# Performance work log

Measured on AMD Instinct MI355X. Metric: run time of the kernel, lower is better.

Reference implementation:

```python
import jax, jax.numpy as jnp
import numpy as np

B, S, D, H, FF = 1, 2048, 2048, 32, 8192
HD = D // H
SCALING = HD ** -0.5
WBITS, ABITS = 8, 8
NEG = jnp.finfo(jnp.float32).min


def ste_round(x):
    # straight-through estimator round
    return x + jax.lax.stop_gradient(jnp.round(x) - x)


def fake_quant(x, bits, axis):
    # min-max asymmetric fake quantization (OmniQuant-style dynamic quant)
    qmax = float(2 ** bits - 1)
    xmin = jnp.minimum(jnp.min(x, axis=axis, keepdims=True), 0.0)
    xmax = jnp.maximum(jnp.max(x, axis=axis, keepdims=True), 0.0)
    scale = jnp.maximum((xmax - xmin) / qmax, 1e-5)
    zp = jnp.round(-xmin / scale)
    q = jnp.clip(ste_round(x / scale) + zp, 0.0, qmax)
    return (q - zp) * scale


def qlinear(x, W, b):
    # QuantLinear: quantize activation per-token, weight per-output-channel
    xq = fake_quant(x, ABITS, -1)
    Wq = fake_quant(W, WBITS, 1)  # W: [out, in], per-row (output channel)
    return xq @ Wq.T + b


def layernorm(x, g, b):
    mu = jnp.mean(x, axis=-1, keepdims=True)
    var = jnp.var(x, axis=-1, keepdims=True)
    return (x - mu) * jax.lax.rsqrt(var + 1e-5) * g + b


def setup_inputs():
    key = jax.random.key(0)
    ks = jax.random.split(key, 16)
    w = lambda k, shape: (jax.random.normal(k, shape) * 0.02).astype(jnp.float32)
    hidden_states = jax.random.normal(ks[0], (B, S, D), dtype=jnp.float32)
    causal = jnp.tril(jnp.ones((S, S), dtype=bool))
    attention_mask = jnp.where(causal, 0.0, NEG)[None, None].astype(jnp.float32)
    attention_mask = jnp.broadcast_to(attention_mask, (B, 1, S, S))
    return {
        'hidden_states': hidden_states,
        'attention_mask': attention_mask,
        'Wq': w(ks[1], (D, D)), 'bq': jnp.zeros((D,), jnp.float32),
        'Wk': w(ks[2], (D, D)), 'bk': jnp.zeros((D,), jnp.float32),
        'Wv': w(ks[3], (D, D)), 'bv': jnp.zeros((D,), jnp.float32),
        'Wo': w(ks[4], (D, D)), 'bo': jnp.zeros((D,), jnp.float32),
        'ln1_g': jnp.ones((D,), jnp.float32), 'ln1_b': jnp.zeros((D,), jnp.float32),
        'W1': w(ks[5], (FF, D)), 'b1': jnp.zeros((FF,), jnp.float32),
        'W2': w(ks[6], (D, FF)), 'b2': jnp.zeros((D,), jnp.float32),
        'ln2_g': jnp.ones((D,), jnp.float32), 'ln2_b': jnp.zeros((D,), jnp.float32),
    }


def _split_heads(x):
    # [B,S,D] -> [B,H,S,HD]
    return x.reshape(B, S, H, HD).transpose(0, 2, 1, 3)


def _layer(hidden_states, attention_mask, Wq, bq, Wk, bk, Wv, bv, Wo, bo,
           ln1_g, ln1_b, W1, b1, W2, b2, ln2_g, ln2_b):
    # ---- self attention block (do_layer_norm_before=True) ----
    residual = hidden_states
    x = layernorm(hidden_states, ln1_g, ln1_b)

    q = qlinear(x, Wq, bq) * SCALING
    q = fake_quant(q, ABITS, -1)          # qkt_matmul.quant_x1
    k = qlinear(x, Wk, bk)
    k = fake_quant(k, ABITS, -1)          # qkt_matmul.quant_x2
    v = qlinear(x, Wv, bv)
    v = fake_quant(v, ABITS, -1)          # pv_matmul.quant_x2

    qh, kh, vh = _split_heads(q), _split_heads(k), _split_heads(v)
    scores = jnp.einsum('bhqd,bhkd->bhqk', qh, kh)  # [B,H,S,S]
    scores = scores + attention_mask
    scores = jnp.maximum(scores, NEG)
    probs = jax.nn.softmax(scores, axis=-1)
    probs = fake_quant(probs, ABITS, -1)  # pv_matmul.quant_x1
    ctx = jnp.einsum('bhqk,bhkd->bhqd', probs, vh)
    ctx = ctx.transpose(0, 2, 1, 3).reshape(B, S, D)
    attn_out = qlinear(ctx, Wo, bo)
    hidden_states = residual + attn_out

    # ---- FFN block ----
    residual = hidden_states
    x = layernorm(hidden_states, ln2_g, ln2_b)
    x = jax.nn.relu(qlinear(x, W1, b1))
    x = qlinear(x, W2, b2)
    return residual + x


def reference(hidden_states, attention_mask, Wq, bq, Wk, bk, Wv, bv, Wo, bo,
              ln1_g, ln1_b, W1, b1, W2, b2, ln2_g, ln2_b):
    return _layer(hidden_states, attention_mask, Wq, bq, Wk, bk, Wv, bv, Wo, bo,
                  ln1_g, ln1_b, W1, b1, W2, b2, ln2_g, ln2_b)
```

## Files before the change

### kernel.cpp

```cpp
#include <hip/hip_runtime.h>
#include <hip/hip_bf16.h>
#include <math.h>

#define S_LEN 2048
#define D_DIM 2048
#define H_NUM 32
#define HD_DIM 64
#define FF_DIM 8192
#define QMAX 255.0f

typedef __attribute__((ext_vector_type(4))) float f32x4;
typedef __attribute__((ext_vector_type(4))) int i32x4;
typedef __attribute__((ext_vector_type(8))) __bf16 bf16x8;
typedef unsigned short u16;
typedef signed char i8;

__device__ __forceinline__ u16 f32i_to_bf16(float v) {
  return (u16)(__float_as_uint(v) >> 16);
}
__device__ __forceinline__ u16 f32_to_bf16_rne(float v) {
  __bf16 b = (__bf16)v;
  return *(u16*)&b;
}
__device__ __forceinline__ float bf16_to_f32(u16 u) {
  return __uint_as_float((unsigned int)u << 16);
}
__device__ __forceinline__ int pack4_i8(float q0, float q1, float q2, float q3) {
  int c0 = (int)q0 - 128, c1 = (int)q1 - 128, c2 = (int)q2 - 128, c3 = (int)q3 - 128;
  return (c0 & 0xFF) | ((c1 & 0xFF) << 8) | ((c2 & 0xFF) << 16) | ((c3 & 0xFF) << 24);
}

__device__ __forceinline__ float wred_sum(float v) {
#pragma unroll
  for (int o = 1; o < 64; o <<= 1) v += __shfl_xor(v, o, 64);
  return v;
}
__device__ __forceinline__ float wred_min(float v) {
#pragma unroll
  for (int o = 1; o < 64; o <<= 1) v = fminf(v, __shfl_xor(v, o, 64));
  return v;
}
__device__ __forceinline__ float wred_max(float v) {
#pragma unroll
  for (int o = 1; o < 64; o <<= 1) v = fmaxf(v, __shfl_xor(v, o, 64));
  return v;
}

__device__ __forceinline__ void gload_lds16(const void* g, void* l) {
  __builtin_amdgcn_global_load_lds(
      (__attribute__((address_space(1))) void*)(g),
      (__attribute__((address_space(3))) void*)(l), 16, 0, 0);
}

__device__ __forceinline__ void xcd_swz(int& bx, int& by) {
  const int gx = gridDim.x;
  const int nwg = gx * gridDim.y;
  const int orig = blockIdx.x + gx * blockIdx.y;
  const int swz = (orig & 7) * (nwg >> 3) + (orig >> 3);
  bx = swz % gx;
  by = swz / gx;
}

__global__ __launch_bounds__(256) void ln_quant_i8(const float* __restrict__ x,
                                                   const float* __restrict__ g,
                                                   const float* __restrict__ bvec,
                                                   i8* __restrict__ out,
                                                   float* __restrict__ srow,
                                                   float* __restrict__ zrow,
                                                   float* __restrict__ S0row,
                                                   float* __restrict__ S1row) {
  __shared__ float red[8];
  const int row = blockIdx.x, tid = threadIdx.x;
  const float4* xr = (const float4*)(x + (size_t)row * D_DIM);
  const float4* g4 = (const float4*)g;
  const float4* b4 = (const float4*)bvec;

  float4 v0 = xr[tid], v1 = xr[tid + 256];
  float s = v0.x + v0.y + v0.z + v0.w + v1.x + v1.y + v1.z + v1.w;
  float ss = v0.x * v0.x + v0.y * v0.y + v0.z * v0.z + v0.w * v0.w +
             v1.x * v1.x + v1.y * v1.y + v1.z * v1.z + v1.w * v1.w;
  s = wred_sum(s); ss = wred_sum(ss);
  if ((tid & 63) == 0) { red[tid >> 6] = s; red[4 + (tid >> 6)] = ss; }
  __syncthreads();
  float mu = (red[0] + red[1] + red[2] + red[3]) / (float)D_DIM;
  float var = (red[4] + red[5] + red[6] + red[7]) / (float)D_DIM - mu * mu;
  float rstd = 1.0f / sqrtf(var + 1e-5f);
  __syncthreads();

  float mn = 0.f, mx = 0.f;
  float4 n0, n1;
  {
    float4 gg = g4[tid], bb = b4[tid];
    n0.x = (v0.x - mu) * rstd * gg.x + bb.x; n0.y = (v0.y - mu) * rstd * gg.y + bb.y;
    n0.z = (v0.z - mu) * rstd * gg.z + bb.z; n0.w = (v0.w - mu) * rstd * gg.w + bb.w;
    gg = g4[tid + 256]; bb = b4[tid + 256];
    n1.x = (v1.x - mu) * rstd * gg.x + bb.x; n1.y = (v1.y - mu) * rstd * gg.y + bb.y;
    n1.z = (v1.z - mu) * rstd * gg.z + bb.z; n1.w = (v1.w - mu) * rstd * gg.w + bb.w;
    mn = fminf(mn, fminf(fminf(n0.x, n0.y), fminf(n0.z, n0.w)));
    mn = fminf(mn, fminf(fminf(n1.x, n1.y), fminf(n1.z, n1.w)));
    mx = fmaxf(mx, fmaxf(fmaxf(n0.x, n0.y), fmaxf(n0.z, n0.w)));
    mx = fmaxf(mx, fmaxf(fmaxf(n1.x, n1.y), fmaxf(n1.z, n1.w)));
  }
  mn = wred_min(mn); mx = wred_max(mx);
  if ((tid & 63) == 0) { red[tid >> 6] = mn; red[4 + (tid >> 6)] = mx; }
  __syncthreads();
  mn = fminf(fminf(red[0], red[1]), fminf(red[2], red[3]));
  mx = fmaxf(fmaxf(red[4], red[5]), fmaxf(red[6], red[7]));
  float scale = fmaxf((mx - mn) / QMAX, 1e-5f);
  float zp = rintf(-mn / scale);
  if (tid == 0) { srow[row] = scale; zrow[row] = 128.0f - zp; }

  float q00 = fminf(fmaxf(rintf(n0.x / scale) + zp, 0.f), QMAX);
  float q01 = fminf(fmaxf(rintf(n0.y / scale) + zp, 0.f), QMAX);
  float q02 = fminf(fmaxf(rintf(n0.z / scale) + zp, 0.f), QMAX);
  float q03 = fminf(fmaxf(rintf(n0.w / scale) + zp, 0.f), QMAX);
  float q10 = fminf(fmaxf(rintf(n1.x / scale) + zp, 0.f), QMAX);
  float q11 = fminf(fmaxf(rintf(n1.y / scale) + zp, 0.f), QMAX);
  float q12 = fminf(fmaxf(rintf(n1.z / scale) + zp, 0.f), QMAX);
  float q13 = fminf(fmaxf(rintf(n1.w / scale) + zp, 0.f), QMAX);
  *(int*)&out[(size_t)row * D_DIM + tid * 4] = pack4_i8(q00, q01, q02, q03);
  *(int*)&out[(size_t)row * D_DIM + 1024 + tid * 4] = pack4_i8(q10, q11, q12, q13);
  float s0 = q00 + q01 + q02 + q03 - 512.f;
  float s1 = q10 + q11 + q12 + q13 - 512.f;
  __syncthreads();
  s0 = wred_sum(s0); s1 = wred_sum(s1);
  if ((tid & 63) == 0) { red[tid >> 6] = s0; red[4 + (tid >> 6)] = s1; }
  __syncthreads();
  if (tid == 0) {
    S0row[row] = red[0] + red[1] + red[2] + red[3];
    S1row[row] = red[4] + red[5] + red[6] + red[7];
  }
}

__global__ __launch_bounds__(256) void act_quant_i8(const float* __restrict__ x,
                                                    i8* __restrict__ out,
                                                    float* __restrict__ srow,
                                                    float* __restrict__ zrow,
                                                    float* __restrict__ S0row,
                                                    float* __restrict__ S1row) {
  __shared__ float red[8];
  const int row = blockIdx.x, tid = threadIdx.x;
  const float4* xr = (const float4*)(x + (size_t)row * D_DIM);
  float4 n0 = xr[tid], n1 = xr[tid + 256];
  float mn = 0.f, mx = 0.f;
  mn = fminf(mn, fminf(fminf(n0.x, n0.y), fminf(n0.z, n0.w)));
  mn = fminf(mn, fminf(fminf(n1.x, n1.y), fminf(n1.z, n1.w)));
  mx = fmaxf(mx, fmaxf(fmaxf(n0.x, n0.y), fmaxf(n0.z, n0.w)));
  mx = fmaxf(mx, fmaxf(fmaxf(n1.x, n1.y), fmaxf(n1.z, n1.w)));
  mn = wred_min(mn); mx = wred_max(mx);
  if ((tid & 63) == 0) { red[tid >> 6] = mn; red[4 + (tid >> 6)] = mx; }
  __syncthreads();
  mn = fminf(fminf(red[0], red[1]), fminf(red[2], red[3]));
  mx = fmaxf(fmaxf(red[4], red[5]), fmaxf(red[6], red[7]));
  float scale = fmaxf((mx - mn) / QMAX, 1e-5f);
  float zp = rintf(-mn / scale);
  if (tid == 0) { srow[row] = scale; zrow[row] = 128.0f - zp; }
  float q00 = fminf(fmaxf(rintf(n0.x / scale) + zp, 0.f), QMAX);
  float q01 = fminf(fmaxf(rintf(n0.y / scale) + zp, 0.f), QMAX);
  float q02 = fminf(fmaxf(rintf(n0.z / scale) + zp, 0.f), QMAX);
  float q03 = fminf(fmaxf(rintf(n0.w / scale) + zp, 0.f), QMAX);
  float q10 = fminf(fmaxf(rintf(n1.x / scale) + zp, 0.f), QMAX);
  float q11 = fminf(fmaxf(rintf(n1.y / scale) + zp, 0.f), QMAX);
  float q12 = fminf(fmaxf(rintf(n1.z / scale) + zp, 0.f), QMAX);
  float q13 = fminf(fmaxf(rintf(n1.w / scale) + zp, 0.f), QMAX);
  *(int*)&out[(size_t)row * D_DIM + tid * 4] = pack4_i8(q00, q01, q02, q03);
  *(int*)&out[(size_t)row * D_DIM + 1024 + tid * 4] = pack4_i8(q10, q11, q12, q13);
  float s0 = q00 + q01 + q02 + q03 - 512.f;
  float s1 = q10 + q11 + q12 + q13 - 512.f;
  __syncthreads();
  s0 = wred_sum(s0); s1 = wred_sum(s1);
  if ((tid & 63) == 0) { red[tid >> 6] = s0; red[4 + (tid >> 6)] = s1; }
  __syncthreads();
  if (tid == 0) {
    S0row[row] = red[0] + red[1] + red[2] + red[3];
    S1row[row] = red[4] + red[5] + red[6] + red[7];
  }
}

__device__ __forceinline__ void wquant_body(const float* __restrict__ wr0,
                                            i8* __restrict__ wo,
                                            float* __restrict__ sc,
                                            float* __restrict__ zc,
                                            float* __restrict__ S0c,
                                            float* __restrict__ S1c,
                                            int row, int K) {
  __shared__ float red[8];
  const int tid = threadIdx.x;
  const float4* wr = (const float4*)wr0;
  const int K4 = K >> 2, H4 = K4 >> 1;
  float mn = 0.f, mx = 0.f;
  for (int i = tid; i < K4; i += 256) {
    float4 v = wr[i];
    mn = fminf(mn, fminf(fminf(v.x, v.y), fminf(v.z, v.w)));
    mx = fmaxf(mx, fmaxf(fmaxf(v.x, v.y), fmaxf(v.z, v.w)));
  }
  mn = wred_min(mn); mx = wred_max(mx);
  if ((tid & 63) == 0) { red[tid >> 6] = mn; red[4 + (tid >> 6)] = mx; }
  __syncthreads();
  mn = fminf(fminf(red[0], red[1]), fminf(red[2], red[3]));
  mx = fmaxf(fmaxf(red[4], red[5]), fmaxf(red[6], red[7]));
  float scale = fmaxf((mx - mn) / QMAX, 1e-5f);
  float zp = rintf(-mn / scale);
  if (tid == 0) { sc[row] = scale; zc[row] = 128.0f - zp; }
  float s0 = 0.f, s1 = 0.f;
  for (int i = tid; i < K4; i += 256) {
    float4 v = wr[i];
    float q0 = fminf(fmaxf(rintf(v.x / scale) + zp, 0.f), QMAX);
    float q1 = fminf(fmaxf(rintf(v.y / scale) + zp, 0.f), QMAX);
    float q2 = fminf(fmaxf(rintf(v.z / scale) + zp, 0.f), QMAX);
    float q3 = fminf(fmaxf(rintf(v.w / scale) + zp, 0.f), QMAX);
    *(int*)&wo[i * 4] = pack4_i8(q0, q1, q2, q3);
    float gs = q0 + q1 + q2 + q3 - 512.f;
    if (i < H4) s0 += gs; else s1 += gs;
  }
  __syncthreads();
  s0 = wred_sum(s0); s1 = wred_sum(s1);
  if ((tid & 63) == 0) { red[tid >> 6] = s0; red[4 + (tid >> 6)] = s1; }
  __syncthreads();
  if (tid == 0) {
    S0c[row] = red[0] + red[1] + red[2] + red[3];
    S1c[row] = red[4] + red[5] + red[6] + red[7];
  }
}

__global__ __launch_bounds__(256) void wquant_i8(const float* __restrict__ W,
                                                 i8* __restrict__ Wi,
                                                 float* __restrict__ sc,
                                                 float* __restrict__ zc,
                                                 float* __restrict__ S0c,
                                                 float* __restrict__ S1c, int K) {
  const int row = blockIdx.x;
  wquant_body(W + (size_t)row * K, Wi + (size_t)row * K, sc, zc, S0c, S1c, row, K);
}

__global__ __launch_bounds__(256) void wquant4_i8(
    const float* __restrict__ W0, i8* __restrict__ O0, float* s0, float* z0, float* a0, float* b0,
    const float* __restrict__ W1, i8* __restrict__ O1, float* s1, float* z1, float* a1, float* b1,
    const float* __restrict__ W2, i8* __restrict__ O2, float* s2, float* z2, float* a2, float* b2,
    const float* __restrict__ W3, i8* __restrict__ O3, float* s3, float* z3, float* a3, float* b3) {
  const int which = blockIdx.x >> 11;
  const int row = blockIdx.x & (D_DIM - 1);
  const float* W = (which == 0) ? W0 : (which == 1) ? W1 : (which == 2) ? W2 : W3;
  i8* O = (which == 0) ? O0 : (which == 1) ? O1 : (which == 2) ? O2 : O3;
  float* sc = (which == 0) ? s0 : (which == 1) ? s1 : (which == 2) ? s2 : s3;
  float* zc = (which == 0) ? z0 : (which == 1) ? z1 : (which == 2) ? z2 : z3;
  float* Sa = (which == 0) ? a0 : (which == 1) ? a1 : (which == 2) ? a2 : a3;
  float* Sb = (which == 0) ? b0 : (which == 1) ? b1 : (which == 2) ? b2 : b3;
  wquant_body(W + (size_t)row * D_DIM, O + (size_t)row * D_DIM, sc, zc, Sa, Sb, row, D_DIM);
}

__global__ __launch_bounds__(256) void requant3(
    const u16* __restrict__ qv, const float* __restrict__ tqmn, const float* __restrict__ tqmx,
    u16* __restrict__ qo, float* __restrict__ sqv,
    const u16* __restrict__ kv, const float* __restrict__ tkmn, const float* __restrict__ tkmx,
    u16* __restrict__ ko, float* __restrict__ skv,
    const u16* __restrict__ vv, const float* __restrict__ tvmn, const float* __restrict__ tvmx,
    u16* __restrict__ vo) {
  __shared__ float red[8];
  const int wh = blockIdx.x >> 11;
  const int row = blockIdx.x & (S_LEN - 1);
  const int tid = threadIdx.x;
  const u16* vals = (wh == 0) ? qv : (wh == 1) ? kv : vv;
  const float* tmn = (wh == 0) ? tqmn : (wh == 1) ? tkmn : tvmn;
  const float* tmx = (wh == 0) ? tqmx : (wh == 1) ? tkmx : tvmx;
  u16* out = (wh == 0) ? qo : (wh == 1) ? ko : vo;
  float* srow = (wh == 0) ? sqv : (wh == 1) ? skv : nullptr;
  const int value_mode = (wh == 2) ? 1 : 0;

  float mn = 0.f, mx = 0.f;
  if (tid < 32) {
    mn = tmn[(size_t)row * 32 + tid];
    mx = tmx[(size_t)row * 32 + tid];
  }
  mn = wred_min(mn); mx = wred_max(mx);
  if ((tid & 63) == 0) { red[tid >> 6] = mn; red[4 + (tid >> 6)] = mx; }
  __syncthreads();
  mn = fminf(fminf(red[0], red[1]), fminf(red[2], red[3]));
  mx = fmaxf(fmaxf(red[4], red[5]), fmaxf(red[6], red[7]));
  mn = fminf(mn, 0.f); mx = fmaxf(mx, 0.f);
  float scale = fmaxf((mx - mn) / QMAX, 1e-5f);
  float zp = rintf(-mn / scale);
  if (srow && tid == 0) srow[row] = scale;
  const ushort4* vr = (const ushort4*)(vals + (size_t)row * D_DIM);
  ushort4* orow = (ushort4*)(out + (size_t)row * D_DIM);
  for (int i = tid; i < D_DIM / 4; i += 256) {
    ushort4 u = vr[i];
    float q0 = fminf(fmaxf(rintf(bf16_to_f32(u.x) / scale) + zp, 0.f), QMAX) - zp;
    float q1 = fminf(fmaxf(rintf(bf16_to_f32(u.y) / scale) + zp, 0.f), QMAX) - zp;
    float q2 = fminf(fmaxf(rintf(bf16_to_f32(u.z) / scale) + zp, 0.f), QMAX) - zp;
    float q3 = fminf(fmaxf(rintf(bf16_to_f32(u.w) / scale) + zp, 0.f), QMAX) - zp;
    ushort4 o;
    if (value_mode) {
      o.x = f32_to_bf16_rne(q0 * scale); o.y = f32_to_bf16_rne(q1 * scale);
      o.z = f32_to_bf16_rne(q2 * scale); o.w = f32_to_bf16_rne(q3 * scale);
    } else {
      o.x = f32i_to_bf16(q0); o.y = f32i_to_bf16(q1);
      o.z = f32i_to_bf16(q2); o.w = f32i_to_bf16(q3);
    }
    orow[i] = o;
  }
}

__global__ __launch_bounds__(256) void requant_ff_i8(const u16* __restrict__ vals,
                                                     const float* __restrict__ tmx,
                                                     i8* __restrict__ out,
                                                     float* __restrict__ srow,
                                                     float* __restrict__ zrow,
                                                     float* __restrict__ S0row,
                                                     float* __restrict__ S1row) {
  __shared__ float red[8];
  const int row = blockIdx.x, tid = threadIdx.x;
  float mx = (tid < 128) ? tmx[(size_t)row * 128 + tid] : 0.f;
  mx = wred_max(mx);
  if ((tid & 63) == 0) red[tid >> 6] = mx;
  __syncthreads();
  mx = fmaxf(fmaxf(red[0], red[1]), fmaxf(red[2], red[3]));
  mx = fmaxf(mx, 0.f);
  float scale = fmaxf(mx / QMAX, 1e-5f);
  if (tid == 0) { srow[row] = scale; zrow[row] = 128.0f; }
  const ushort4* vr = (const ushort4*)(vals + (size_t)row * FF_DIM);
  const int N4 = FF_DIM >> 2;
  float s0 = 0.f, s1 = 0.f;
  for (int i = tid; i < N4; i += 256) {
    ushort4 u = vr[i];
    float q0 = fminf(fmaxf(rintf(bf16_to_f32(u.x) / scale), 0.f), QMAX);
    float q1 = fminf(fmaxf(rintf(bf16_to_f32(u.y) / scale), 0.f), QMAX);
    float q2 = fminf(fmaxf(rintf(bf16_to_f32(u.z) / scale), 0.f), QMAX);
    float q3 = fminf(fmaxf(rintf(bf16_to_f32(u.w) / scale), 0.f), QMAX);
    *(int*)&out[(size_t)row * FF_DIM + i * 4] = pack4_i8(q0, q1, q2, q3);
    float gs = q0 + q1 + q2 + q3 - 512.f;
    if (i < 1024) s0 += gs; else s1 += gs;
  }
  __syncthreads();
  s0 = wred_sum(s0); s1 = wred_sum(s1);
  if ((tid & 63) == 0) { red[tid >> 6] = s0; red[4 + (tid >> 6)] = s1; }
  __syncthreads();
  if (tid == 0) {
    S0row[row] = red[0] + red[1] + red[2] + red[3];
    S1row[row] = red[4] + red[5] + red[6] + red[7];
  }
}

__device__ __forceinline__ void gemm128_i8_db(
    const i8* __restrict__ A, const i8* __restrict__ B,
    int K, int bm, int bn, int k_begin, int k_end,
    i8* As, i8* Bs, i32x4 (&acc)[4][4]) {
  const int tid = threadIdx.x;
  const int wid = tid >> 6, lane = tid & 63;
  const int wr = wid >> 1, wc = wid & 1;
  const int lr = lane & 15, lk = lane >> 4;
  const int r0 = tid >> 2, c0 = (tid & 3) * 16;
  const int r1 = 64 + r0;
  const size_t ldsb0 = (size_t)(wid * 64) * 16;
  const size_t ldsb1 = (size_t)(256 + wid * 64) * 16;

  const i8* Ag0 = A + (size_t)(bm + r0) * K + c0;
  const i8* Ag1 = A + (size_t)(bm + r1) * K + c0;
  const i8* Bg0 = B + (size_t)(bn + r0) * K + c0;
  const i8* Bg1 = B + (size_t)(bn + r1) * K + c0;

  const int nt = (k_end - k_begin) >> 6;

#define STAGE_I8(t)                                   \
  {                                                   \
    const int _k = k_begin + (t) * 64;                \
    i8* _Ab = As + (size_t)((t) & 1) * 8192;          \
    i8* _Bb = Bs + (size_t)((t) & 1) * 8192;          \
    gload_lds16(Ag0 + _k, _Ab + ldsb0);               \
    gload_lds16(Ag1 + _k, _Ab + ldsb1);               \
    gload_lds16(Bg0 + _k, _Bb + ldsb0);               \
    gload_lds16(Bg1 + _k, _Bb + ldsb1);               \
  }

  STAGE_I8(0);
  __syncthreads();

  for (int t = 0; t < nt; ++t) {
    const i8* Ac = As + (size_t)(t & 1) * 8192;
    const i8* Bc = Bs + (size_t)(t & 1) * 8192;
    i32x4 af[4], bf[4];
#pragma unroll
    for (int mi = 0; mi < 4; ++mi)
      af[mi] = *(const i32x4*)&Ac[(size_t)(wr * 64 + mi * 16 + lr) * 64 + lk * 16];
#pragma unroll
    for (int ni = 0; ni < 4; ++ni)
      bf[ni] = *(const i32x4*)&Bc[(size_t)(wc * 64 + ni * 16 + lr) * 64 + lk * 16];
    if (t + 1 < nt) STAGE_I8(t + 1);
#pragma unroll
    for (int mi = 0; mi < 4; ++mi)
#pragma unroll
      for (int ni = 0; ni < 4; ++ni)
        acc[mi][ni] = __builtin_amdgcn_mfma_i32_16x16x64_i8(af[mi], bf[ni], acc[mi][ni], 0, 0, 0);
    __syncthreads();
  }
#undef STAGE_I8
}

__global__ __launch_bounds__(256) void gemm_qkv_i8(
    const i8* __restrict__ A, const float* __restrict__ sx, const float* __restrict__ zx,
    const float* __restrict__ Sx0, const float* __restrict__ Sx1,
    const i8* __restrict__ Bq, const float* __restrict__ sbq, const float* __restrict__ zbq,
    const float* __restrict__ Sq0, const float* __restrict__ Sq1,
    const float* __restrict__ biasq, u16* __restrict__ Cq,
    float* __restrict__ tqmn, float* __restrict__ tqmx,
    const i8* __restrict__ Bk, const float* __restrict__ sbk, const float* __restrict__ zbk,
    const float* __restrict__ Sk0, const float* __restrict__ Sk1,
    const float* __restrict__ biask, u16* __restrict__ Ck,
    float* __restrict__ tkmn, float* __restrict__ tkmx,
    const i8* __restrict__ Bv, const float* __restrict__ sbv, const float* __restrict__ zbv,
    const float* __restrict__ Sv0, const float* __restrict__ Sv1,
    const float* __restrict__ biasv, u16* __restrict__ Cv,
    float* __restrict__ tvmn, float* __restrict__ tvmx) {
  __shared__ __align__(16) i8 As[2 * 128 * 64], Bs[2 * 128 * 64];
  int bx, by; xcd_swz(bx, by);
  const int which = bx >> 4;
  const int bn = (bx & 15) * 128;
  const int bm = by * 128;
  const i8* B = (which == 0) ? Bq : (which == 1) ? Bk : Bv;
  const float* sb = (which == 0) ? sbq : (which == 1) ? sbk : sbv;
  const float* zb = (which == 0) ? zbq : (which == 1) ? zbk : zbv;
  const float* Sb0 = (which == 0) ? Sq0 : (which == 1) ? Sk0 : Sv0;
  const float* Sb1 = (which == 0) ? Sq1 : (which == 1) ? Sk1 : Sv1;
  const float* bias = (which == 0) ? biasq : (which == 1) ? biask : biasv;
  u16* C = (which == 0) ? Cq : (which == 1) ? Ck : Cv;
  float* tmn = (which == 0) ? tqmn : (which == 1) ? tkmn : tvmn;
  float* tmx = (which == 0) ? tqmx : (which == 1) ? tkmx : tvmx;
  const float alpha = (which == 0) ? 0.125f : 1.0f;

  i32x4 acc[4][4] = {};
  gemm128_i8_db(A, B, D_DIM, bm, bn, 0, D_DIM, As, Bs, acc);

  const int tid = threadIdx.x;
  const int wid = tid >> 6, lane = tid & 63;
  const int wr = wid >> 1, wc = wid & 1;
  const int lr = lane & 15, lk = lane >> 4;
  const int col0 = bn + wc * 64 + lr;
  const int rbase = bm + wr * 64 + lk * 4;
  const int tci = (bn >> 6) + wc;
  float sbc[4], zbc[4], Sbc[4], bc[4];
#pragma unroll
  for (int ni = 0; ni < 4; ++ni) {
    const int col = col0 + ni * 16;
    sbc[ni] = sb[col]; zbc[ni] = zb[col];
    Sbc[ni] = Sb0[col] + Sb1[col]; bc[ni] = bias[col];
  }
#pragma unroll
  for (int mi = 0; mi < 4; ++mi) {
#pragma unroll
    for (int r = 0; r < 4; ++r) {
      const int row = rbase + mi * 16 + r;
      const float sar = sx[row], zar = zx[row];
      const float Sar = Sx0[row] + Sx1[row];
// ... 99 lines not shown
#pragma unroll
    for (int mi = 0; mi < 4; ++mi)
#pragma unroll
      for (int r = 0; r < 4; ++r)
        dst[(size_t)(rbase + mi * 16 + r) * D_DIM + col] = (float)acc[mi][ni][r];
  }
}

__global__ __launch_bounds__(256) void splitk_reduce4(
    const float* __restrict__ part,
    const float* __restrict__ sxa, const float* __restrict__ zxa,
    const float* __restrict__ Sxa0, const float* __restrict__ Sxa1,
    const float* __restrict__ sw, const float* __restrict__ zw,
    const float* __restrict__ Sw0, const float* __restrict__ Sw1,
    float Kf, const float* __restrict__ bias, const float* __restrict__ res,
    float* __restrict__ out) {
  const size_t st4 = (size_t)S_LEN * D_DIM / 4;
  for (size_t i = (size_t)blockIdx.x * 256 + threadIdx.x; i < st4;
       i += (size_t)gridDim.x * 256) {
    const int row = (int)(i >> 9);
    const int c4 = (int)(i & 511);
    float4 s = ((const float4*)part)[i];
    float4 p1 = ((const float4*)part)[i + st4];
    float4 p2 = ((const float4*)part)[i + 2 * st4];
    float4 p3 = ((const float4*)part)[i + 3 * st4];
    s.x += p1.x + p2.x + p3.x; s.y += p1.y + p2.y + p3.y;
    s.z += p1.z + p2.z + p3.z; s.w += p1.w + p2.w + p3.w;
    const float sxr = sxa[row], zxr = zxa[row];
    const float Sxr = Sxa0[row] + Sxa1[row];
    float4 ws = ((const float4*)sw)[c4];
    float4 wz = ((const float4*)zw)[c4];
    float4 w0 = ((const float4*)Sw0)[c4];
    float4 w1 = ((const float4*)Sw1)[c4];
    float4 b4 = ((const float4*)bias)[c4];
    float4 o;
    o.x = sxr * ws.x * (s.x + zxr * (w0.x + w1.x) + wz.x * Sxr + Kf * zxr * wz.x) + b4.x;
    o.y = sxr * ws.y * (s.y + zxr * (w0.y + w1.y) + wz.y * Sxr + Kf * zxr * wz.y) + b4.y;
    o.z = sxr * ws.z * (s.z + zxr * (w0.z + w1.z) + wz.z * Sxr + Kf * zxr * wz.z) + b4.z;
    o.w = sxr * ws.w * (s.w + zxr * (w0.w + w1.w) + wz.w * Sxr + Kf * zxr * wz.w) + b4.w;
    if (res) {
      float4 r = ((const float4*)res)[i];
      o.x += r.x; o.y += r.y; o.z += r.z; o.w += r.w;
    }
    ((float4*)out)[i] = o;
  }
}

__global__ __launch_bounds__(256) void splitk_reduce_ln(
    const float* __restrict__ part,
    const float* __restrict__ sxa, const float* __restrict__ zxa,
    const float* __restrict__ Sxa0, const float* __restrict__ Sxa1,
    const float* __restrict__ sw, const float* __restrict__ zw,
    const float* __restrict__ Sw0, const float* __restrict__ Sw1,
    const float* __restrict__ bias, const float* __restrict__ res,
    float* __restrict__ h2out,
    const float* __restrict__ g, const float* __restrict__ bvec,
    i8* __restrict__ out, float* __restrict__ srow, float* __restrict__ zrow,
    float* __restrict__ S0row, float* __restrict__ S1row) {
  __shared__ float red[8];
  const int row = blockIdx.x, tid = threadIdx.x;
  const size_t st = (size_t)S_LEN * D_DIM;
  const float4* p0 = (const float4*)(part + (size_t)row * D_DIM);
  const float4* p1 = (const float4*)(part + st + (size_t)row * D_DIM);
  const float4* p2 = (const float4*)(part + 2 * st + (size_t)row * D_DIM);
  const float4* p3 = (const float4*)(part + 3 * st + (size_t)row * D_DIM);
  const float4* rr = (const float4*)(res + (size_t)row * D_DIM);
  const float4* b4 = (const float4*)bias;
  const float4* g4 = (const float4*)g;
  const float4* e4 = (const float4*)bvec;

  const float sxr = sxa[row], zxr = zxa[row];
  const float Sxr = Sxa0[row] + Sxa1[row];

  float4 v0, v1;
#pragma unroll
  for (int h = 0; h < 2; ++h) {
    const int idx = tid + h * 256;
    float4 a = p0[idx], q = p1[idx], u = p2[idx], w = p3[idx];
    float4 ws = ((const float4*)sw)[idx];
    float4 wz = ((const float4*)zw)[idx];
    float4 s0 = ((const float4*)Sw0)[idx];
    float4 s1 = ((const float4*)Sw1)[idx];
    float4 bb = b4[idx], rv = rr[idx];
    float4 o;
    o.x = sxr * ws.x * (a.x + q.x + u.x + w.x + zxr * (s0.x + s1.x) + wz.x * Sxr + 2048.0f * zxr * wz.x) + bb.x + rv.x;
    o.y = sxr * ws.y * (a.y + q.y + u.y + w.y + zxr * (s0.y + s1.y) + wz.y * Sxr + 2048.0f * zxr * wz.y) + bb.y + rv.y;
    o.z = sxr * ws.z * (a.z + q.z + u.z + w.z + zxr * (s0.z + s1.z) + wz.z * Sxr + 2048.0f * zxr * wz.z) + bb.z + rv.z;
    o.w = sxr * ws.w * (a.w + q.w + u.w + w.w + zxr * (s0.w + s1.w) + wz.w * Sxr + 2048.0f * zxr * wz.w) + bb.w + rv.w;
    if (h == 0) v0 = o; else v1 = o;
  }
  float* h2r = h2out + (size_t)row * D_DIM;
  *(float4*)&h2r[tid * 4] = v0;
  *(float4*)&h2r[1024 + tid * 4] = v1;

  float s = v0.x + v0.y + v0.z + v0.w + v1.x + v1.y + v1.z + v1.w;
  float ss = v0.x * v0.x + v0.y * v0.y + v0.z * v0.z + v0.w * v0.w +
             v1.x * v1.x + v1.y * v1.y + v1.z * v1.z + v1.w * v1.w;
  s = wred_sum(s); ss = wred_sum(ss);
  if ((tid & 63) == 0) { red[tid >> 6] = s; red[4 + (tid >> 6)] = ss; }
  __syncthreads();
  float mu = (red[0] + red[1] + red[2] + red[3]) / (float)D_DIM;
  float var = (red[4] + red[5] + red[6] + red[7]) / (float)D_DIM - mu * mu;
  float rstd = 1.0f / sqrtf(var + 1e-5f);
  __syncthreads();

  float mn = 0.f, mx = 0.f;
  float4 n0, n1;
  {
    float4 gg = g4[tid], bb = e4[tid];
    n0.x = (v0.x - mu) * rstd * gg.x + bb.x; n0.y = (v0.y - mu) * rstd * gg.y + bb.y;
    n0.z = (v0.z - mu) * rstd * gg.z + bb.z; n0.w = (v0.w - mu) * rstd * gg.w + bb.w;
    gg = g4[tid + 256]; bb = e4[tid + 256];
    n1.x = (v1.x - mu) * rstd * gg.x + bb.x; n1.y = (v1.y - mu) * rstd * gg.y + bb.y;
    n1.z = (v1.z - mu) * rstd * gg.z + bb.z; n1.w = (v1.w - mu) * rstd * gg.w + bb.w;
    mn = fminf(mn, fminf(fminf(n0.x, n0.y), fminf(n0.z, n0.w)));
    mn = fminf(mn, fminf(fminf(n1.x, n1.y), fminf(n1.z, n1.w)));
    mx = fmaxf(mx, fmaxf(fmaxf(n0.x, n0.y), fmaxf(n0.z, n0.w)));
    mx = fmaxf(mx, fmaxf(fmaxf(n1.x, n1.y), fmaxf(n1.z, n1.w)));
  }
  mn = wred_min(mn); mx = wred_max(mx);
  if ((tid & 63) == 0) { red[tid >> 6] = mn; red[4 + (tid >> 6)] = mx; }
  __syncthreads();
  mn = fminf(fminf(red[0], red[1]), fminf(red[2], red[3]));
  mx = fmaxf(fmaxf(red[4], red[5]), fmaxf(red[6], red[7]));
  float scale = fmaxf((mx - mn) / QMAX, 1e-5f);
  float zp = rintf(-mn / scale);
  if (tid == 0) { srow[row] = scale; zrow[row] = 128.0f - zp; }
  float q00 = fminf(fmaxf(rintf(n0.x / scale) + zp, 0.f), QMAX);
  float q01 = fminf(fmaxf(rintf(n0.y / scale) + zp, 0.f), QMAX);
  float q02 = fminf(fmaxf(rintf(n0.z / scale) + zp, 0.f), QMAX);
  float q03 = fminf(fmaxf(rintf(n0.w / scale) + zp, 0.f), QMAX);
  float q10 = fminf(fmaxf(rintf(n1.x / scale) + zp, 0.f), QMAX);
  float q11 = fminf(fmaxf(rintf(n1.y / scale) + zp, 0.f), QMAX);
  float q12 = fminf(fmaxf(rintf(n1.z / scale) + zp, 0.f), QMAX);
  float q13 = fminf(fmaxf(rintf(n1.w / scale) + zp, 0.f), QMAX);
  *(int*)&out[(size_t)row * D_DIM + tid * 4] = pack4_i8(q00, q01, q02, q03);
  *(int*)&out[(size_t)row * D_DIM + 1024 + tid * 4] = pack4_i8(q10, q11, q12, q13);
  float s0 = q00 + q01 + q02 + q03 - 512.f;
  float s1 = q10 + q11 + q12 + q13 - 512.f;
  __syncthreads();
  s0 = wred_sum(s0); s1 = wred_sum(s1);
  if ((tid & 63) == 0) { red[tid >> 6] = s0; red[4 + (tid >> 6)] = s1; }
  __syncthreads();
  if (tid == 0) {
    S0row[row] = red[0] + red[1] + red[2] + red[3];
    S1row[row] = red[4] + red[5] + red[6] + red[7];
  }
}

__global__ __launch_bounds__(256) void attn_ml(
    const u16* __restrict__ qi, const float* __restrict__ sq,
    const u16* __restrict__ ki, const float* __restrict__ sk,
    float* __restrict__ Mb, float* __restrict__ Lb) {
  __shared__ __align__(16) u16 Qs[64][72];
  __shared__ __align__(16) u16 Ks[64][72];
  const int bid = blockIdx.x;
  const int ti = (S_LEN / 64 - 1) - (bid >> 5);
  const int h = bid & (H_NUM - 1);
  const int i0 = ti * 64;
  const int tid = threadIdx.x;
  const int wid = tid >> 6, lane = tid & 63;
  const int lr = lane & 15, g = lane >> 4;
  const size_t hbase = (size_t)h * HD_DIM;

  const int r_a = tid >> 3, ch_a = tid & 7;
  const int r_b = 32 + r_a;

  for (int c = tid; c < 512; c += 256) {
    int r = c >> 3, ch = c & 7;
    *(float4*)&Qs[r][ch * 8] =
        *(const float4*)&qi[(size_t)(i0 + r) * D_DIM + hbase + ch * 8];
  }
  float sq4[4];
#pragma unroll
  for (int r = 0; r < 4; ++r) sq4[r] = sq[i0 + wid * 16 + g * 4 + r];
  __syncthreads();

  const int ntiles = i0 / 64 + 1;
  float m_r[4] = {-1e30f, -1e30f, -1e30f, -1e30f};
  float l_r[4] = {0.f, 0.f, 0.f, 0.f};

  float4 ka0 = *(const float4*)&ki[(size_t)r_a * D_DIM + hbase + ch_a * 8];
  float4 ka1 = *(const float4*)&ki[(size_t)r_b * D_DIM + hbase + ch_a * 8];
  for (int t = 0; t < ntiles; ++t) {
    __syncthreads();
    *(float4*)&Ks[r_a][ch_a * 8] = ka0;
    *(float4*)&Ks[r_b][ch_a * 8] = ka1;
    __syncthreads();
    if (t + 1 < ntiles) {
      const int jn = (t + 1) * 64;
      ka0 = *(const float4*)&ki[(size_t)(jn + r_a) * D_DIM + hbase + ch_a * 8];
      ka1 = *(const float4*)&ki[(size_t)(jn + r_b) * D_DIM + hbase + ch_a * 8];
    }

    bf16x8 aq0 = *(const bf16x8*)&Qs[wid * 16 + lr][g * 8];
    bf16x8 aq1 = *(const bf16x8*)&Qs[wid * 16 + lr][32 + g * 8];
    f32x4 accs[4] = {};
#pragma unroll
    for (int ni = 0; ni < 4; ++ni) {
      bf16x8 b0 = *(const bf16x8*)&Ks[ni * 16 + lr][g * 8];
      bf16x8 b1 = *(const bf16x8*)&Ks[ni * 16 + lr][32 + g * 8];
      accs[ni] = __builtin_amdgcn_mfma_f32_16x16x32_bf16(aq0, b0, accs[ni], 0, 0, 0);
      accs[ni] = __builtin_amdgcn_mfma_f32_16x16x32_bf16(aq1, b1, accs[ni], 0, 0, 0);
    }

    const int jt = t * 64;
    float sv[4][4];
#pragma unroll
    for (int ni = 0; ni < 4; ++ni) {
      const float skc = sk[jt + ni * 16 + lr];
#pragma unroll
      for (int r = 0; r < 4; ++r) sv[ni][r] = accs[ni][r] * sq4[r] * skc;
    }
    if (t == ntiles - 1) {
      const int jcol = jt + lr, irow = i0 + wid * 16 + g * 4;
#pragma unroll
      for (int ni = 0; ni < 4; ++ni)
#pragma unroll
        for (int r = 0; r < 4; ++r)
          if (jcol + ni * 16 > irow + r) sv[ni][r] = -1e30f;
    }
#pragma unroll
    for (int r = 0; r < 4; ++r) {
      float tmax = fmaxf(fmaxf(sv[0][r], sv[1][r]), fmaxf(sv[2][r], sv[3][r]));
      tmax = fmaxf(tmax, __shfl_xor(tmax, 1, 64));
      tmax = fmaxf(tmax, __shfl_xor(tmax, 2, 64));
      tmax = fmaxf(tmax, __shfl_xor(tmax, 4, 64));
      tmax = fmaxf(tmax, __shfl_xor(tmax, 8, 64));
      float mnew = fmaxf(m_r[r], tmax);
      float sum = __expf(sv[0][r] - mnew) + __expf(sv[1][r] - mnew) +
                  __expf(sv[2][r] - mnew) + __expf(sv[3][r] - mnew);
      sum += __shfl_xor(sum, 1, 64);
      sum += __shfl_xor(sum, 2, 64);
      sum += __shfl_xor(sum, 4, 64);
      sum += __shfl_xor(sum, 8, 64);
      l_r[r] = l_r[r] * __expf(m_r[r] - mnew) + sum;
      m_r[r] = mnew;
    }
  }

  if (lr == 0) {
#pragma unroll
    for (int r = 0; r < 4; ++r) {
      const int row = i0 + wid * 16 + g * 4 + r;
      Mb[(size_t)h * S_LEN + row] = m_r[r];
      Lb[(size_t)h * S_LEN + row] = l_r[r];
    }
  }
}

__global__ __launch_bounds__(256) void attn_pv(
    const u16* __restrict__ qi, const float* __restrict__ sq,
    const u16* __restrict__ ki, const float* __restrict__ sk,
    const u16* __restrict__ vf,
    const float* __restrict__ Mb, const float* __restrict__ Lb,
    float* __restrict__ ctx) {
  __shared__ __align__(16) u16 Qs[64][72];
  __shared__ __align__(16) u16 Ks[64][72];
  __shared__ __align__(16) u16 Ps[64][72];
  __shared__ __align__(16) u16 Vt[64][72];
  const int bid = blockIdx.x;
  const int ti = (S_LEN / 64 - 1) - (bid >> 5);
  const int h = bid & (H_NUM - 1);
  const int i0 = ti * 64;
  const int tid = threadIdx.x;
  const int wid = tid >> 6, lane = tid & 63;
  const int lr = lane & 15, g = lane >> 4;
  const size_t hbase = (size_t)h * HD_DIM;

  const int r_a = tid >> 3, ch_a = tid & 7;
  const int r_b = 32 + r_a;
  const int jr_v = tid & 63, ch_v = tid >> 6;

  for (int c = tid; c < 512; c += 256) {
    int r = c >> 3, ch = c & 7;
    *(float4*)&Qs[r][ch * 8] =
        *(const float4*)&qi[(size_t)(i0 + r) * D_DIM + hbase + ch * 8];
  }
  float sq4[4], m_r[4], qsc[4], idn[4];
#pragma unroll
  for (int r = 0; r < 4; ++r) {
    const int row = i0 + wid * 16 + g * 4 + r;
    sq4[r] = sq[row];
    m_r[r] = Mb[(size_t)h * S_LEN + row];
    float li = Lb[(size_t)h * S_LEN + row];
    float sc = fmaxf((1.0f / li) / QMAX, 1e-5f);
    qsc[r] = sc;
    idn[r] = 1.0f / (li * sc);
  }
  __syncthreads();

  const int ntiles = i0 / 64 + 1;
  f32x4 acco[4] = {};
  float4 kb0 = *(const float4*)&ki[(size_t)r_a * D_DIM + hbase + ch_a * 8];
  float4 kb1 = *(const float4*)&ki[(size_t)r_b * D_DIM + hbase + ch_a * 8];
  float4 vb0 = *(const float4*)&vf[(size_t)jr_v * D_DIM + hbase + ch_v * 8];
  float4 vb1 = *(const float4*)&vf[(size_t)jr_v * D_DIM + hbase + (4 + ch_v) * 8];
  for (int t = 0; t < ntiles; ++t) {
    __syncthreads();
    *(float4*)&Ks[r_a][ch_a * 8] = kb0;
    *(float4*)&Ks[r_b][ch_a * 8] = kb1;
    {
      const u16* v0 = (const u16*)&vb0;
      const u16* v1 = (const u16*)&vb1;
#pragma unroll
      for (int e = 0; e < 8; ++e) Vt[ch_v * 8 + e][jr_v] = v0[e];
#pragma unroll
      for (int e = 0; e < 8; ++e) Vt[(4 + ch_v) * 8 + e][jr_v] = v1[e];
    }
    __syncthreads();
    if (t + 1 < ntiles) {
      const int jn = (t + 1) * 64;
      kb0 = *(const float4*)&ki[(size_t)(jn + r_a) * D_DIM + hbase + ch_a * 8];
      kb1 = *(const float4*)&ki[(size_t)(jn + r_b) * D_DIM + hbase + ch_a * 8];
      vb0 = *(const float4*)&vf[(size_t)(jn + jr_v) * D_DIM + hbase + ch_v * 8];
      vb1 = *(const float4*)&vf[(size_t)(jn + jr_v) * D_DIM + hbase + (4 + ch_v) * 8];
    }

    bf16x8 aq0 = *(const bf16x8*)&Qs[wid * 16 + lr][g * 8];
    bf16x8 aq1 = *(const bf16x8*)&Qs[wid * 16 + lr][32 + g * 8];
    f32x4 accs[4] = {};
#pragma unroll
    for (int ni = 0; ni < 4; ++ni) {
      bf16x8 b0 = *(const bf16x8*)&Ks[ni * 16 + lr][g * 8];
      bf16x8 b1 = *(const bf16x8*)&Ks[ni * 16 + lr][32 + g * 8];
      accs[ni] = __builtin_amdgcn_mfma_f32_16x16x32_bf16(aq0, b0, accs[ni], 0, 0, 0);
      accs[ni] = __builtin_amdgcn_mfma_f32_16x16x32_bf16(aq1, b1, accs[ni], 0, 0, 0);
    }

    const int jt = t * 64;
    const bool diag = (t == ntiles - 1);
    const int jcol = jt + lr, irow = i0 + wid * 16 + g * 4;
#pragma unroll
    for (int ni = 0; ni < 4; ++ni) {
      const float skc = sk[jt + ni * 16 + lr];
#pragma unroll
      for (int r = 0; r < 4; ++r) {
        float s = accs[ni][r] * sq4[r] * skc;
        if (diag && (jcol + ni * 16 > irow + r)) s = -1e30f;
        float e = __expf(s - m_r[r]);
        float q8 = fminf(fmaxf(rintf(e * idn[r]), 0.f), QMAX);
        Ps[wid * 16 + g * 4 + r][ni * 16 + lr] = f32i_to_bf16(q8);
      }
    }

    bf16x8 ap0 = *(const bf16x8*)&Ps[wid * 16 + lr][g * 8];
    bf16x8 ap1 = *(const bf16x8*)&Ps[wid * 16 + lr][32 + g * 8];
#pragma unroll
    for (int ni = 0; ni < 4; ++ni) {
      bf16x8 b0 = *(const bf16x8*)&Vt[ni * 16 + lr][g * 8];
      bf16x8 b1 = *(const bf16x8*)&Vt[ni * 16 + lr][32 + g * 8];
      acco[ni] = __builtin_amdgcn_mfma_f32_16x16x32_bf16(ap0, b0, acco[ni], 0, 0, 0);
      acco[ni] = __builtin_amdgcn_mfma_f32_16x16x32_bf16(ap1, b1, acco[ni], 0, 0, 0);
    }
  }

#pragma unroll
  for (int ni = 0; ni < 4; ++ni)
#pragma unroll
    for (int r = 0; r < 4; ++r) {
      const int row = i0 + wid * 16 + g * 4 + r;
      ctx[(size_t)row * D_DIM + hbase + ni * 16 + lr] = acco[ni][r] * qsc[r];
    }
}

extern "C" void kernel_launch(void* const* d_in, const int* in_sizes, int n_in,
                              void* d_out, int out_size, void* d_ws, size_t ws_size,
                              hipStream_t stream) {
  (void)in_sizes; (void)n_in; (void)out_size;
  const float* hs  = (const float*)d_in[0];
  const float* Wq  = (const float*)d_in[2];
  const float* bq  = (const float*)d_in[3];
  const float* Wk  = (const float*)d_in[4];
  const float* bk  = (const float*)d_in[5];
  const float* Wv  = (const float*)d_in[6];
  const float* bv  = (const float*)d_in[7];
  const float* Wo  = (const float*)d_in[8];
  const float* bo  = (const float*)d_in[9];
  const float* g1  = (const float*)d_in[10];
  const float* be1 = (const float*)d_in[11];
  const float* W1  = (const float*)d_in[12];
  const float* bf1 = (const float*)d_in[13];
  const float* W2  = (const float*)d_in[14];
  const float* bf2 = (const float*)d_in[15];
  const float* g2  = (const float*)d_in[16];
  const float* be2 = (const float*)d_in[17];
  float* out = (float*)d_out;

  const size_t SD = (size_t)S_LEN * D_DIM;
  const size_t SF = (size_t)S_LEN * FF_DIM;
  const size_t HS = (size_t)H_NUM * S_LEN;

  char* p = (char*)d_ws;
  auto alloc = [&](size_t bytes) { char* r = p; p += (bytes + 255) & ~(size_t)255; return r; };

  float* h2   = (float*)alloc(SD * 4);
  float* sx   = (float*)alloc(S_LEN * 4);
  float* zx   = (float*)alloc(S_LEN * 4);
  float* Sx0  = (float*)alloc(S_LEN * 4);
  float* Sx1  = (float*)alloc(S_LEN * 4);
  float* sy   = (float*)alloc(S_LEN * 4);
  float* zy   = (float*)alloc(S_LEN * 4);
  float* Sy0  = (float*)alloc(S_LEN * 4);
  float* Sy1  = (float*)alloc(S_LEN * 4);
  float* sxf  = (float*)alloc(S_LEN * 4);
  float* zxf  = (float*)alloc(S_LEN * 4);
  float* Sf0  = (float*)alloc(S_LEN * 4);
  float* Sf1  = (float*)alloc(S_LEN * 4);
  float* sqv  = (float*)alloc(S_LEN * 4);
  float* skv  = (float*)alloc(S_LEN * 4);
  float* Mb   = (float*)alloc(HS * 4);
  float* Lbv  = (float*)alloc(HS * 4);
  float* swq = (float*)alloc(D_DIM * 4); float* zwq = (float*)alloc(D_DIM * 4);
  float* Sq0 = (float*)alloc(D_DIM * 4); float* Sq1 = (float*)alloc(D_DIM * 4);
  float* swk = (float*)alloc(D_DIM * 4); float* zwk = (float*)alloc(D_DIM * 4);
  float* Sk0 = (float*)alloc(D_DIM * 4); float* Sk1 = (float*)alloc(D_DIM * 4);
  float* swv = (float*)alloc(D_DIM * 4); float* zwv = (float*)alloc(D_DIM * 4);
  float* Sv0 = (float*)alloc(D_DIM * 4); float* Sv1 = (float*)alloc(D_DIM * 4);
  float* swo = (float*)alloc(D_DIM * 4); float* zwo = (float*)alloc(D_DIM * 4);
  float* So0 = (float*)alloc(D_DIM * 4); float* So1 = (float*)alloc(D_DIM * 4);
  float* sw1 = (float*)alloc(FF_DIM * 4); float* zw1 = (float*)alloc(FF_DIM * 4);
  float* S10 = (float*)alloc(FF_DIM * 4); float* S11 = (float*)alloc(FF_DIM * 4);
  float* sw2 = (float*)alloc(D_DIM * 4); float* zw2 = (float*)alloc(D_DIM * 4);
  float* S20 = (float*)alloc(D_DIM * 4); float* S21 = (float*)alloc(D_DIM * 4);
  float* tqmn = (float*)alloc(S_LEN * 32 * 4);
  float* tqmx = (float*)alloc(S_LEN * 32 * 4);
  float* tkmn = (float*)alloc(S_LEN * 32 * 4);
  float* tkmx = (float*)alloc(S_LEN * 32 * 4);
  float* tvmn = (float*)alloc(S_LEN * 32 * 4);
  float* tvmx = (float*)alloc(S_LEN * 32 * 4);
  float* tf1x = (float*)alloc(S_LEN * 128 * 4);
  i8* xi  = (i8*)alloc(SD);
  i8* wqi = (i8*)alloc(SD);
  i8* wki = (i8*)alloc(SD);
  i8* wvi = (i8*)alloc(SD);
  i8* woi = (i8*)alloc(SD);
  i8* w1i = (i8*)alloc(SF);
  i8* w2i = (i8*)alloc(SF);
  i8* f1i = (i8*)alloc(SF);
  char* arena = alloc(8 * SD * 2);
  u16* qv   = (u16*)arena;
  u16* kv   = qv + SD;
  u16* vv   = kv + SD;
  u16* qi8  = vv + SD;
  u16* ki8  = qi8 + SD;
  u16* vfb  = ki8 + SD;
  float* ctxb = (float*)(vfb + SD);
  float* pwo = (float*)arena;
  u16* f1v = (u16*)arena;
  float* pw2 = (float*)arena;
  size_t need = (size_t)(p - (char*)d_ws);
  if (ws_size < need) return;

  dim3 blk(256);

  wquant4_i8<<<4 * D_DIM, blk, 0, stream>>>(
      Wq, wqi, swq, zwq, Sq0, Sq1,
      Wk, wki, swk, zwk, Sk0, Sk1,
      Wv, wvi, swv, zwv, Sv0, Sv1,
      Wo, woi, swo, zwo, So0, So1);
  wquant_i8<<<FF_DIM, blk, 0, stream>>>(W1, w1i, sw1, zw1, S10, S11, D_DIM);
  wquant_i8<<<D_DIM, blk, 0, stream>>>(W2, w2i, sw2, zw2, S20, S21, FF_DIM);

  ln_quant_i8<<<S_LEN, blk, 0, stream>>>(hs, g1, be1, xi, sx, zx, Sx0, Sx1);

  dim3 gqkv(3 * D_DIM / 128, S_LEN / 128);
  gemm_qkv_i8<<<gqkv, blk, 0, stream>>>(xi, sx, zx, Sx0, Sx1,
                                        wqi, swq, zwq, Sq0, Sq1, bq, qv, tqmn, tqmx,
                                        wki, swk, zwk, Sk0, Sk1, bk, kv, tkmn, tkmx,
                                        wvi, swv, zwv, Sv0, Sv1, bv, vv, tvmn, tvmx);

  requant3<<<3 * S_LEN, blk, 0, stream>>>(qv, tqmn, tqmx, qi8, sqv,
                                          kv, tkmn, tkmx, ki8, skv,
                                          vv, tvmn, tvmx, vfb);

  const int ga = (S_LEN / 64) * H_NUM;
  attn_ml<<<ga, blk, 0, stream>>>(qi8, sqv, ki8, skv, Mb, Lbv);
  attn_pv<<<ga, blk, 0, stream>>>(qi8, sqv, ki8, skv, vfb, Mb, Lbv, ctxb);

  act_quant_i8<<<S_LEN, blk, 0, stream>>>(ctxb, xi, sx, zx, Sx0, Sx1);

  dim3 gwo(D_DIM / 128, S_LEN / 128, 4);
  gemm_splitk_i8<<<gwo, blk, 0, stream>>>(xi, woi, pwo, D_DIM, 4);
  splitk_reduce_ln<<<S_LEN, blk, 0, stream>>>(pwo, sx, zx, Sx0, Sx1,
                                              swo, zwo, So0, So1, bo, hs, h2,
                                              g2, be2, xi, sy, zy, Sy0, Sy1);

  dim3 gff(FF_DIM / 128, S_LEN / 128);
  gemm_w1_i8<<<gff, blk, 0, stream>>>(xi, sy, zy, Sy0, Sy1,
                                      w1i, sw1, zw1, S10, S11, bf1, f1v, tf1x);
  requant_ff_i8<<<S_LEN, blk, 0, stream>>>(f1v, tf1x, f1i, sxf, zxf, Sf0, Sf1);

  dim3 gw2(D_DIM / 128, S_LEN / 128, 4);
  gemm_splitk_i8<<<gw2, blk, 0, stream>>>(f1i, w2i, pw2, FF_DIM, 4);
  splitk_reduce4<<<2048, blk, 0, stream>>>(pw2, sxf, zxf, Sf0, Sf1,
                                           sw2, zw2, S20, S21, (float)FF_DIM,
                                           bf2, h2, out);
}
```

Before: 421.1 us.

## Pre-transpose V, load Q fragments directly, and use exp2 with folded scales in attention

Adds a separate kernel that transposes the quantized V into a head-major [d][seq] buffer. attn_pv can then fill its Vt shared tile with vectorized stores instead of scattered 2-byte writes. Q fragments are read straight from global into registers, which drops the Qs shared tile and a barrier. The softmax now uses exp2f with log2e folded into the query scale, and the probability normalization is folded into a per-row bias. The cost is an extra kernel launch and a full pass over V, plus small rounding differences from the exp2 rewrite.

```diff
diff --git a/kernel.cpp b/kernel.cpp
--- a/kernel.cpp
+++ b/kernel.cpp
@@ -8,6 +8,7 @@
 #define HD_DIM 64
 #define FF_DIM 8192
 #define QMAX 255.0f
+#define LOG2E 1.4426950408889634f
 
 typedef __attribute__((ext_vector_type(4))) float f32x4;
 typedef __attribute__((ext_vector_type(4))) int i32x4;
@@ -298,6 +299,27 @@
       o.z = f32i_to_bf16(q2); o.w = f32i_to_bf16(q3);
     }
     orow[i] = o;
+  }
+}
+
+__global__ __launch_bounds__(256) void transpose_v(const u16* __restrict__ vfb,
+                                                   u16* __restrict__ vtb) {
+  __shared__ u16 Ts[64][66];
+  const int j0 = blockIdx.x * 64;
+  const int h = blockIdx.y;
+  const int tid = threadIdx.x;
+  for (int c = tid; c < 512; c += 256) {
+    int r = c >> 3, ch = c & 7;
+    *(float4*)&Ts[r][ch * 8] =
+        *(const float4*)&vfb[(size_t)(j0 + r) * D_DIM + h * HD_DIM + ch * 8];
+  }
+  __syncthreads();
+  for (int c = tid; c < 512; c += 256) {
+    int d = c >> 3, ch = c & 7;
+    u16 tmp[8];
+#pragma unroll
+    for (int e = 0; e < 8; ++e) tmp[e] = Ts[ch * 8 + e][d];
+    *(float4*)&vtb[(size_t)(h * HD_DIM + d) * S_LEN + j0 + ch * 8] = *(float4*)tmp;
   }
 }
 
@@ -703,7 +725,6 @@
     const u16* __restrict__ qi, const float* __restrict__ sq,
     const u16* __restrict__ ki, const float* __restrict__ sk,
     float* __restrict__ Mb, float* __restrict__ Lb) {
-  __shared__ __align__(16) u16 Qs[64][72];
   __shared__ __align__(16) u16 Ks[64][72];
   const int bid = blockIdx.x;
   const int ti = (S_LEN / 64 - 1) - (bid >> 5);
@@ -717,15 +738,11 @@
   const int r_a = tid >> 3, ch_a = tid & 7;
   const int r_b = 32 + r_a;
 
-  for (int c = tid; c < 512; c += 256) {
-    int r = c >> 3, ch = c & 7;
-    *(float4*)&Qs[r][ch * 8] =
-        *(const float4*)&qi[(size_t)(i0 + r) * D_DIM + hbase + ch * 8];
-  }
-  float sq4[4];
-#pragma unroll
-  for (int r = 0; r < 4; ++r) sq4[r] = sq[i0 + wid * 16 + g * 4 + r];
-  __syncthreads();
+  const bf16x8 aq0 = *(const bf16x8*)&qi[(size_t)(i0 + wid * 16 + lr) * D_DIM + hbase + g * 8];
+  const bf16x8 aq1 = *(const bf16x8*)&qi[(size_t)(i0 + wid * 16 + lr) * D_DIM + hbase + 32 + g * 8];
+  float sq2[4];
+#pragma unroll
+  for (int r = 0; r < 4; ++r) sq2[r] = sq[i0 + wid * 16 + g * 4 + r] * LOG2E;
 
   const int ntiles = i0 / 64 + 1;
   float m_r[4] = {-1e30f, -1e30f, -1e30f, -1e30f};
@@ -744,8 +761,6 @@
       ka1 = *(const float4*)&ki[(size_t)(jn + r_b) * D_DIM + hbase + ch_a * 8];
     }
 
-    bf16x8 aq0 = *(const bf16x8*)&Qs[wid * 16 + lr][g * 8];
-    bf16x8 aq1 = *(const bf16x8*)&Qs[wid * 16 + lr][32 + g * 8];
     f32x4 accs[4] = {};
 #pragma unroll
     for (int ni = 0; ni < 4; ++ni) {
@@ -756,12 +771,12 @@
     }
 
     const int jt = t * 64;
-    float sv[4][4];
+    float tv[4][4];
 #pragma unroll
     for (int ni = 0; ni < 4; ++ni) {
       const float skc = sk[jt + ni * 16 + lr];
 #pragma unroll
-      for (int r = 0; r < 4; ++r) sv[ni][r] = accs[ni][r] * sq4[r] * skc;
+      for (int r = 0; r < 4; ++r) tv[ni][r] = accs[ni][r] * sq2[r] * skc;
     }
     if (t == ntiles - 1) {
       const int jcol = jt + lr, irow = i0 + wid * 16 + g * 4;
@@ -769,23 +784,23 @@
       for (int ni = 0; ni < 4; ++ni)
 #pragma unroll
         for (int r = 0; r < 4; ++r)
-          if (jcol + ni * 16 > irow + r) sv[ni][r] = -1e30f;
+          if (jcol + ni * 16 > irow + r) tv[ni][r] = -1e30f;
     }
 #pragma unroll
     for (int r = 0; r < 4; ++r) {
-      float tmax = fmaxf(fmaxf(sv[0][r], sv[1][r]), fmaxf(sv[2][r], sv[3][r]));
+      float tmax = fmaxf(fmaxf(tv[0][r], tv[1][r]), fmaxf(tv[2][r], tv[3][r]));
       tmax = fmaxf(tmax, __shfl_xor(tmax, 1, 64));
       tmax = fmaxf(tmax, __shfl_xor(tmax, 2, 64));
       tmax = fmaxf(tmax, __shfl_xor(tmax, 4, 64));
       tmax = fmaxf(tmax, __shfl_xor(tmax, 8, 64));
       float mnew = fmaxf(m_r[r], tmax);
-      float sum = __expf(sv[0][r] - mnew) + __expf(sv[1][r] - mnew) +
-                  __expf(sv[2][r] - mnew) + __expf(sv[3][r] - mnew);
+      float sum = exp2f(tv[0][r] - mnew) + exp2f(tv[1][r] - mnew) +
+                  exp2f(tv[2][r] - mnew) + exp2f(tv[3][r] - mnew);
       sum += __shfl_xor(sum, 1, 64);
       sum += __shfl_xor(sum, 2, 64);
       sum += __shfl_xor(sum, 4, 64);
       sum += __shfl_xor(sum, 8, 64);
-      l_r[r] = l_r[r] * __expf(m_r[r] - mnew) + sum;
+      l_r[r] = l_r[r] * exp2f(m_r[r] - mnew) + sum;
       m_r[r] = mnew;
     }
   }
@@ -803,10 +818,9 @@
 __global__ __launch_bounds__(256) void attn_pv(
     const u16* __restrict__ qi, const float* __restrict__ sq,
     const u16* __restrict__ ki, const float* __restrict__ sk,
-    const u16* __restrict__ vf,
+    const u16* __restrict__ vt,
     const float* __restrict__ Mb, const float* __restrict__ Lb,
     float* __restrict__ ctx) {
-  __shared__ __align__(16) u16 Qs[64][72];
   __shared__ __align__(16) u16 Ks[64][72];
   __shared__ __align__(16) u16 Ps[64][72];
   __shared__ __align__(16) u16 Vt[64][72];
@@ -818,58 +832,47 @@
   const int wid = tid >> 6, lane = tid & 63;
   const int lr = lane & 15, g = lane >> 4;
   const size_t hbase = (size_t)h * HD_DIM;
+  const size_t vtbase = (size_t)h * HD_DIM * S_LEN;
 
   const int r_a = tid >> 3, ch_a = tid & 7;
   const int r_b = 32 + r_a;
-  const int jr_v = tid & 63, ch_v = tid >> 6;
-
-  for (int c = tid; c < 512; c += 256) {
-    int r = c >> 3, ch = c & 7;
-    *(float4*)&Qs[r][ch * 8] =
-        *(const float4*)&qi[(size_t)(i0 + r) * D_DIM + hbase + ch * 8];
-  }
-  float sq4[4], m_r[4], qsc[4], idn[4];
+
+  const bf16x8 aq0 = *(const bf16x8*)&qi[(size_t)(i0 + wid * 16 + lr) * D_DIM + hbase + g * 8];
+  const bf16x8 aq1 = *(const bf16x8*)&qi[(size_t)(i0 + wid * 16 + lr) * D_DIM + hbase + 32 + g * 8];
+
+  float sq2[4], b_r[4], qsc[4];
 #pragma unroll
   for (int r = 0; r < 4; ++r) {
     const int row = i0 + wid * 16 + g * 4 + r;
-    sq4[r] = sq[row];
-    m_r[r] = Mb[(size_t)h * S_LEN + row];
+    sq2[r] = sq[row] * LOG2E;
+    float m_t = Mb[(size_t)h * S_LEN + row];
     float li = Lb[(size_t)h * S_LEN + row];
     float sc = fmaxf((1.0f / li) / QMAX, 1e-5f);
     qsc[r] = sc;
-    idn[r] = 1.0f / (li * sc);
-  }
-  __syncthreads();
+    b_r[r] = m_t - log2f(1.0f / (li * sc));
+  }
 
   const int ntiles = i0 / 64 + 1;
   f32x4 acco[4] = {};
   float4 kb0 = *(const float4*)&ki[(size_t)r_a * D_DIM + hbase + ch_a * 8];
   float4 kb1 = *(const float4*)&ki[(size_t)r_b * D_DIM + hbase + ch_a * 8];
-  float4 vb0 = *(const float4*)&vf[(size_t)jr_v * D_DIM + hbase + ch_v * 8];
-  float4 vb1 = *(const float4*)&vf[(size_t)jr_v * D_DIM + hbase + (4 + ch_v) * 8];
+  float4 vb0 = *(const float4*)&vt[vtbase + (size_t)r_a * S_LEN + ch_a * 8];
+  float4 vb1 = *(const float4*)&vt[vtbase + (size_t)r_b * S_LEN + ch_a * 8];
   for (int t = 0; t < ntiles; ++t) {
     __syncthreads();
     *(float4*)&Ks[r_a][ch_a * 8] = kb0;
     *(float4*)&Ks[r_b][ch_a * 8] = kb1;
-    {
-      const u16* v0 = (const u16*)&vb0;
-      const u16* v1 = (const u16*)&vb1;
-#pragma unroll
-      for (int e = 0; e < 8; ++e) Vt[ch_v * 8 + e][jr_v] = v0[e];
-#pragma unroll
-      for (int e = 0; e < 8; ++e) Vt[(4 + ch_v) * 8 + e][jr_v] = v1[e];
-    }
+    *(float4*)&Vt[r_a][ch_a * 8] = vb0;
+    *(float4*)&Vt[r_b][ch_a * 8] = vb1;
     __syncthreads();
     if (t + 1 < ntiles) {
       const int jn = (t + 1) * 64;
       kb0 = *(const float4*)&ki[(size_t)(jn + r_a) * D_DIM + hbase + ch_a * 8];
       kb1 = *(const float4*)&ki[(size_t)(jn + r_b) * D_DIM + hbase + ch_a * 8];
-      vb0 = *(const float4*)&vf[(size_t)(jn + jr_v) * D_DIM + hbase + ch_v * 8];
-      vb1 = *(const float4*)&vf[(size_t)(jn + jr_v) * D_DIM + hbase + (4 + ch_v) * 8];
-    }
-
-    bf16x8 aq0 = *(const bf16x8*)&Qs[wid * 16 + lr][g * 8];
-    bf16x8 aq1 = *(const bf16x8*)&Qs[wid * 16 + lr][32 + g * 8];
+      vb0 = *(const float4*)&vt[vtbase + (size_t)r_a * S_LEN + jn + ch_a * 8];
+      vb1 = *(const float4*)&vt[vtbase + (size_t)r_b * S_LEN + jn + ch_a * 8];
+    }
+
     f32x4 accs[4] = {};
 #pragma unroll
     for (int ni = 0; ni < 4; ++ni) {
@@ -887,10 +890,9 @@
       const float skc = sk[jt + ni * 16 + lr];
 #pragma unroll
       for (int r = 0; r < 4; ++r) {
-        float s = accs[ni][r] * sq4[r] * skc;
-        if (diag && (jcol + ni * 16 > irow + r)) s = -1e30f;
-        float e = __expf(s - m_r[r]);
-        float q8 = fminf(fmaxf(rintf(e * idn[r]), 0.f), QMAX);
+        float tvv = accs[ni][r] * sq2[r] * skc;
+        if (diag && (jcol + ni * 16 > irow + r)) tvv = -1e30f;
+        float q8 = fminf(rintf(exp2f(tvv - b_r[r])), QMAX);
         Ps[wid * 16 + g * 4 + r][ni * 16 + lr] = f32i_to_bf16(q8);
       }
     }
@@ -997,6 +999,7 @@
   u16* ki8  = qi8 + SD;
   u16* vfb  = ki8 + SD;
   float* ctxb = (float*)(vfb + SD);
+  u16* vtb  = qv;
   float* pwo = (float*)arena;
   u16* f1v = (u16*)arena;
   float* pw2 = (float*)arena;
@@ -1025,9 +1028,12 @@
                                           kv, tkmn, tkmx, ki8, skv,
                                           vv, tvmn, tvmx, vfb);
 
+  dim3 gtv(S_LEN / 64, H_NUM);
+  transpose_v<<<gtv, blk, 0, stream>>>(vfb, vtb);
+
   const int ga = (S_LEN / 64) * H_NUM;
   attn_ml<<<ga, blk, 0, stream>>>(qi8, sqv, ki8, skv, Mb, Lbv);
-  attn_pv<<<ga, blk, 0, stream>>>(qi8, sqv, ki8, skv, vfb, Mb, Lbv, ctxb);
+  attn_pv<<<ga, blk, 0, stream>>>(qi8, sqv, ki8, skv, vtb, Mb, Lbv, ctxb);
 
   act_quant_i8<<<S_LEN, blk, 0, stream>>>(ctxb, xi, sx, zx, Sx0, Sx1);
 
```

After: 420.3 us. Within noise of the previous version (-0.2%).
